# Optimization experiments

Hardware: AMD Instinct MI355X
Metric: run time of the kernel (lower is better)

The kernel has to match this reference:

```python
import jax, jax.numpy as jnp
import numpy as np

N, E, F, H = 50000, 1600000, 128, 128  # nodes, edges, input_nf, hidden_nf


def setup_inputs() -> dict:
    key = jax.random.key(0)
    ks = jax.random.split(key, 16)
    s = 0.05
    inp = {
        "h": jax.random.normal(ks[0], (N, F), jnp.float32),
        "coord": jax.random.normal(ks[1], (N, 3), jnp.float32),
        "edge_index": jax.random.randint(ks[2], (2, E), 0, N, jnp.int32),
        # edge_mlp: Linear(2F+1, H) -> SiLU -> Linear(H, H) -> SiLU
        "We1": jax.random.normal(ks[3], (2 * F + 1, H), jnp.float32) * s,
        "be1": jnp.zeros((H,), jnp.float32),
        "We2": jax.random.normal(ks[4], (H, H), jnp.float32) * s,
        "be2": jnp.zeros((H,), jnp.float32),
        # node_mlp: Linear(H+F, H) -> SiLU -> Linear(H, F)
        "Wn1": jax.random.normal(ks[5], (H + F, H), jnp.float32) * s,
        "bn1": jnp.zeros((H,), jnp.float32),
        "Wn2": jax.random.normal(ks[6], (H, F), jnp.float32) * s,
        "bn2": jnp.zeros((F,), jnp.float32),
        # coord_mlp: Linear(H, H) -> SiLU -> Linear(H, 1, bias=False) (xavier gain 0.001)
        "Wc1": jax.random.normal(ks[7], (H, H), jnp.float32) * s,
        "bc1": jnp.zeros((H,), jnp.float32),
        "Wc2": jax.random.normal(ks[8], (H, 1), jnp.float32) * 0.001,
    }
    return inp


def reference(h, coord, edge_index, We1, be1, We2, be2, Wn1, bn1, Wn2, bn2, Wc1, bc1, Wc2):
    row, col = edge_index[0], edge_index[1]
    n = h.shape[0]

    # coord2radial (normalize=False)
    coord_diff = coord[row] - coord[col]                      # [E, 3]
    radial = jnp.sum(coord_diff * coord_diff, axis=1, keepdims=True)  # [E, 1]

    # edge_model (attention=False, edge_attr=None)
    e_in = jnp.concatenate([h[row], h[col], radial], axis=1)  # [E, 2F+1]
    edge_feat = jax.nn.silu(jax.nn.silu(e_in @ We1 + be1) @ We2 + be2)  # [E, H]

    # coord_model (coords_agg='mean', reflection_equiv=True, tanh=False)
    phi = jax.nn.silu(edge_feat @ Wc1 + bc1) @ Wc2            # [E, 1]
    trans = coord_diff * phi                                   # [E, 3]
    agg_c = jax.ops.segment_sum(trans, row, num_segments=n)    # [N, 3]
    cnt = jax.ops.segment_sum(jnp.ones((trans.shape[0], 1), trans.dtype), row, num_segments=n)
    coord_out = coord + agg_c / jnp.maximum(cnt, 1.0)

    # node_model (node_attr=None, residual=True)
    agg_h = jax.ops.segment_sum(edge_feat, row, num_segments=n)  # [N, H]
    n_in = jnp.concatenate([h, agg_h], axis=1)                   # [N, F+H]
    h_out = h + (jax.nn.silu(n_in @ Wn1 + bn1) @ Wn2 + bn2)

    return h_out, coord_out
```

## Files before the change

kernel.cpp:

```cpp
#include <hip/hip_runtime.h>


typedef float f32x4 __attribute__((ext_vector_type(4)));
typedef short s16x8 __attribute__((ext_vector_type(8)));

#define NN   50000
#define EE   1600000
#define NHF  6400000
#define NBIN 50000
#define NT   25000

__device__ __forceinline__ unsigned short f2bf(float x){
  union { float f; unsigned int u; } v; v.f = x;
  unsigned int r = v.u + 0x7fffu + ((v.u >> 16) & 1u);
  return (unsigned short)(r >> 16);
}
__device__ __forceinline__ unsigned int pack2(float a, float b){
  unsigned int r;
  asm("v_cvt_pk_bf16_f32 %0, %1, %2" : "=v"(r) : "v"(a), "v"(b));
  return r;
}
__device__ __forceinline__ float silu_f(float x){
  return x * __builtin_amdgcn_rcpf(1.f + __expf(-x));
}
__device__ __forceinline__ float bflo(unsigned int u){ return __uint_as_float(u << 16); }
__device__ __forceinline__ float bfhi(unsigned int u){ return __uint_as_float(u & 0xffff0000u); }

__device__ __forceinline__ f32x4 mfma16(s16x8 a, s16x8 b, f32x4 c){
  return __builtin_amdgcn_mfma_f32_16x16x32_bf16(a, b, c, 0, 0, 0);
}

template<int CTRL> __device__ __forceinline__ float dppf(float x){
  return __int_as_float(__builtin_amdgcn_update_dpp(0, __float_as_int(x), CTRL, 0xF, 0xF, true));
}
template<int CTRL> __device__ __forceinline__ int dppi(int x){
  return __builtin_amdgcn_update_dpp(-1, x, CTRL, 0xF, 0xF, false);
}

__device__ __forceinline__ short* sptr(short* base, int fi, int slot){
  return (short*)((char*)base + (fi << 10) + (((slot << 4) ^ ((fi & 3) << 5))));
}

__global__ void pack_weights(const float* __restrict__ We1, const float* __restrict__ We2,
                             const float* __restrict__ Wc1, const float* __restrict__ Wn1,
                             const float* __restrict__ Wn2, short* __restrict__ wp)
{
  int b = blockIdx.x;
  int m = b >> 5, t = b & 31;
  int ft = t >> 2, ks = t & 3;
  int lane = threadIdx.x;
  const float* src;
  switch (m) {
    case 0: src = We1;            break;
    case 1: src = We1 + 128*128;  break;
    case 2: src = We2;            break;
    case 3: src = Wc1;            break;
    case 4: src = Wn1;            break;
    case 5: src = Wn1 + 128*128;  break;
    default: src = Wn2;           break;
  }
  short* dst = wp + m*16384 + (((ft<<2) + ks)*64 + lane)*8;
  int f  = (ft<<4) + (lane & 15);
  int kb = (ks<<5) + ((lane >> 4) << 3);
#pragma unroll
  for (int j = 0; j < 8; ++j)
    dst[j] = (short)f2bf(src[(kb + j)*128 + f]);
}

__global__ __launch_bounds__(256, 2)
void a1_kernel(const float* __restrict__ h32, const short* __restrict__ wp,
               unsigned short* __restrict__ A1)
{
  __shared__ short sA[16][64][8];
  const int tid = threadIdx.x, w = tid >> 6, lane = tid & 63;
  const int n0 = blockIdx.x << 6;
  const int el = tid >> 2, q = tid & 3;
  const int fi0 = ((el >> 4) << 2) + q, er = el & 15;
  {
    const int node = n0 + el;
    if (node < NN) {
      const float* hp = h32 + (size_t)node*128 + q*32;
#pragma unroll
      for (int lg = 0; lg < 4; ++lg) {
        f32x4 u = *(const f32x4*)(hp + lg*8);
        f32x4 v = *(const f32x4*)(hp + lg*8 + 4);
        uint4 o;
        o.x = pack2(u.x, u.y); o.y = pack2(u.z, u.w);
        o.z = pack2(v.x, v.y); o.w = pack2(v.z, v.w);
        *(uint4*)&sA[fi0][lg*16 + er][0] = o;
      }
    } else {
      s16x8 z = {};
#pragma unroll
      for (int lg = 0; lg < 4; ++lg) *(s16x8*)&sA[fi0][lg*16 + er][0] = z;
    }
  }
  __syncthreads();

  static const int wpm[3] = {0, 1, 4};
#pragma unroll
  for (int p = 0; p < 2; ++p) {
    s16x8 af[3][4];
#pragma unroll
    for (int j = 0; j < 3; ++j) {
      const int ftg = w*6 + p*3 + j;
      const int mi = ftg >> 3, fti = ftg & 7;
#pragma unroll
      for (int ks = 0; ks < 4; ++ks)
        af[j][ks] = *(const s16x8*)(wp + wpm[mi]*16384 + (((fti<<2) + ks)*64 + lane)*8);
    }
    f32x4 acc[3][4] = {};
#pragma unroll
    for (int et = 0; et < 4; ++et)
#pragma unroll
      for (int ks = 0; ks < 4; ++ks) {
        s16x8 b = *(const s16x8*)&sA[et*4+ks][lane][0];
#pragma unroll
        for (int j = 0; j < 3; ++j)
          acc[j][et] = mfma16(af[j][ks], b, acc[j][et]);
      }
#pragma unroll
    for (int j = 0; j < 3; ++j) {
      const int ftg = w*6 + p*3 + j;
#pragma unroll
      for (int et = 0; et < 4; ++et) {
        const int node = n0 + et*16 + (lane & 15);
        if (node < NN) {
          f32x4 a = acc[j][et];
          uint2 o; o.x = pack2(a.x, a.y); o.y = pack2(a.z, a.w);
          *(uint2*)(A1 + (size_t)node*384 + ftg*16 + ((lane >> 4) << 2)) = o;
        }
      }
    }
  }
}

__global__ void hist_k(const int* __restrict__ eidx, int* __restrict__ hist)
{
  int e = blockIdx.x*256 + threadIdx.x;
  if (e < EE) atomicAdd(&hist[eidx[e]], 1);
}

__global__ void scan_k(const int* __restrict__ hist, int* __restrict__ cur)
{
  __shared__ int s_a[256];
  const int t = threadIdx.x;
  const int lo = t * 196;
  const int hi = (lo + 196 < NBIN) ? lo + 196 : NBIN;
  int s = 0;
  for (int i = lo; i < hi; ++i) s += hist[i];
  s_a[t] = s;
  __syncthreads();
  int acc = s;
#pragma unroll
  for (int d = 1; d < 256; d <<= 1) {
    int u = (t >= d) ? s_a[t - d] : 0;
    __syncthreads();
    acc += u;
    s_a[t] = acc;
    __syncthreads();
  }
  int run = acc - s;
  for (int i = lo; i < hi; ++i) { cur[i] = run; run += hist[i]; }
}

__global__ void scatter_k(const int* __restrict__ eidx, int* __restrict__ cur,
                          int* __restrict__ perm)
{
  int e = blockIdx.x*256 + threadIdx.x;
  if (e < EE) {
    int p = atomicAdd(&cur[eidx[e]], 1);
    perm[p] = e;
  }
}

__global__ __launch_bounds__(256, 3)
void edge_kernel(const unsigned short* __restrict__ A1, const float* __restrict__ coord,
                 const int* __restrict__ eidx, const int* __restrict__ perm,
                 const short* __restrict__ wp,
                 const float* __restrict__ be1, const float* __restrict__ be2,
                 const float* __restrict__ bc1, const float* __restrict__ We1,
                 const float* __restrict__ Wc2,
                 float* __restrict__ aggh, float* __restrict__ aggc,
                 float* __restrict__ cntb)
{
  __shared__ short sAf[2][16*64*8];
  __shared__ float s_vec[5][128];
  __shared__ float s_rad[64];
  __shared__ float s_cd[64][3];
  __shared__ int   s_ri[64];
  __shared__ int   s_ci[64];
  __shared__ float s_phi[64];

  const int tid  = threadIdx.x;
  const int w    = tid >> 6, lane = tid & 63;
  const int ecol = lane & 15, rgrp = lane >> 4;

  if (tid < 128) {
    s_vec[0][tid] = be1[tid];
    s_vec[1][tid] = be2[tid];
    s_vec[2][tid] = bc1[tid];
    s_vec[3][tid] = We1[256*128 + tid];
    s_vec[4][tid] = Wc2[tid];
  }

  s16x8 wf2[2][4], wf3[2][4];
#pragma unroll
  for (int f2 = 0; f2 < 2; ++f2)
#pragma unroll
    for (int ks = 0; ks < 4; ++ks) {
      wf2[f2][ks] = *(const s16x8*)(wp + 2*16384 + ((((2*w+f2)<<2) + ks)*64 + lane)*8);
      wf3[f2][ks] = *(const s16x8*)(wp + 3*16384 + ((((2*w+f2)<<2) + ks)*64 + lane)*8);
    }

  short* sb0 = &sAf[0][0];
  short* sb1 = &sAf[1][0];

  const int tbeg = blockIdx.x * 13;
  const int tend = (tbeg + 13 < NT) ? tbeg + 13 : NT;

  for (int t = tbeg; t < tend; ++t) {
    const int e0 = t << 6;
    if (tid < 64) {
      int e = perm[e0 + tid];
      int r = eidx[e], c = eidx[EE + e];
      s_ri[tid] = r; s_ci[tid] = c;
      float ax = coord[3*r], ay = coord[3*r+1], az = coord[3*r+2];
      float bx = coord[3*c], by = coord[3*c+1], bz = coord[3*c+2];
      float dx = ax-bx, dy = ay-by, dz = az-bz;
      s_cd[tid][0] = dx; s_cd[tid][1] = dy; s_cd[tid][2] = dz;
      s_rad[tid] = dx*dx + dy*dy + dz*dz;
      s_phi[tid] = 0.f;
    }
    __syncthreads();

    {
      int rr[4], cc[4]; float rd[4];
#pragma unroll
      for (int et = 0; et < 4; ++et) {
        const int e_ = et*16 + ecol;
        rr[et] = s_ri[e_]; cc[et] = s_ci[e_]; rd[et] = s_rad[e_];
      }
      uint2 gr[2][4], gc[2][4];
#pragma unroll
      for (int f2 = 0; f2 < 2; ++f2) {
        const int f0 = (2*w+f2)*16 + (rgrp << 2);
#pragma unroll
        for (int et = 0; et < 4; ++et) {
          gr[f2][et] = *(const uint2*)(A1 + (size_t)rr[et]*384 + f0);
          gc[f2][et] = *(const uint2*)(A1 + (size_t)cc[et]*384 + 128 + f0);
        }
      }
#pragma unroll
      for (int f2 = 0; f2 < 2; ++f2) {
        const int f0 = (2*w+f2)*16 + (rgrp << 2);
        const int ks2 = f0 >> 5, lg2 = (f0 & 31) >> 3, j0 = f0 & 7;
        f32x4 w1c = *(const f32x4*)&s_vec[3][f0];
        f32x4 b1  = *(const f32x4*)&s_vec[0][f0];
#pragma unroll
        for (int et = 0; et < 4; ++et) {
          const uint2 r2v = gr[f2][et], c2v = gc[f2][et];
          f32x4 x;
          x.x = silu_f(bflo(r2v.x) + bflo(c2v.x) + rd[et]*w1c.x + b1.x);
          x.y = silu_f(bfhi(r2v.x) + bfhi(c2v.x) + rd[et]*w1c.y + b1.y);
          x.z = silu_f(bflo(r2v.y) + bflo(c2v.y) + rd[et]*w1c.z + b1.z);
          x.w = silu_f(bfhi(r2v.y) + bfhi(c2v.y) + rd[et]*w1c.w + b1.w);
          uint2 p; p.x = pack2(x.x, x.y); p.y = pack2(x.z, x.w);
          *(uint2*)((char*)sptr(sb0, et*4 + ks2, lg2*16 + ecol) + 2*j0) = p;
        }
      }
    }
    __syncthreads();

    f32x4 a2[2][4] = {};
#pragma unroll
    for (int et = 0; et < 4; ++et)
#pragma unroll
      for (int ks = 0; ks < 4; ++ks) {
        s16x8 b = *(const s16x8*)sptr(sb0, et*4+ks, lane);
        a2[0][et] = mfma16(wf2[0][ks], b, a2[0][et]);
        a2[1][et] = mfma16(wf2[1][ks], b, a2[1][et]);
      }
#pragma unroll
    for (int et = 0; et < 4; ++et) {
      const int r_l = s_ri[et*16 + ecol];
      f32x4 xx0, xx1;
#pragma unroll
      for (int f2 = 0; f2 < 2; ++f2) {
        const int f0 = (2*w+f2)*16 + (rgrp << 2);
        const int ks2 = f0 >> 5, lg2 = (f0 & 31) >> 3, j0 = f0 & 7;
        f32x4 b2 = *(const f32x4*)&s_vec[1][f0];
        f32x4 x = a2[f2][et];
        x.x = silu_f(x.x + b2.x); x.y = silu_f(x.y + b2.y);
        x.z = silu_f(x.z + b2.z); x.w = silu_f(x.w + b2.w);
        uint2 p; p.x = pack2(x.x, x.y); p.y = pack2(x.z, x.w);
        *(uint2*)((char*)sptr(sb1, et*4 + ks2, lg2*16 + ecol) + 2*j0) = p;
        if (f2 == 0) xx0 = x; else xx1 = x;
      }
#define SEG_ROUND(CTRL) { \
      int rn = dppi<CTRL>(r_l); \
      bool ok = (rn == r_l); \
      float u; \
      u = dppf<CTRL>(xx0.x); xx0.x += ok ? u : 0.f; \
      u = dppf<CTRL>(xx0.y); xx0.y += ok ? u : 0.f; \
      u = dppf<CTRL>(xx0.z); xx0.z += ok ? u : 0.f; \
      u = dppf<CTRL>(xx0.w); xx0.w += ok ? u : 0.f; \
      u = dppf<CTRL>(xx1.x); xx1.x += ok ? u : 0.f; \
      u = dppf<CTRL>(xx1.y); xx1.y += ok ? u : 0.f; \
      u = dppf<CTRL>(xx1.z); xx1.z += ok ? u : 0.f; \
      u = dppf<CTRL>(xx1.w); xx1.w += ok ? u : 0.f; }
      SEG_ROUND(0x101)
      SEG_ROUND(0x102)
      SEG_ROUND(0x104)
      SEG_ROUND(0x108)
#undef SEG_ROUND
      const int rprev = dppi<0x111>(r_l);
      if (rprev != r_l) {
        const int f0a = (2*w+0)*16 + (rgrp << 2);
        const int f0b = (2*w+1)*16 + (rgrp << 2);
        float* aga = aggh + (size_t)r_l*128 + f0a;
        float* agb = aggh + (size_t)r_l*128 + f0b;
        atomicAdd(aga+0, xx0.x); atomicAdd(aga+1, xx0.y);
        atomicAdd(aga+2, xx0.z); atomicAdd(aga+3, xx0.w);
        atomicAdd(agb+0, xx1.x); atomicAdd(agb+1, xx1.y);
        atomicAdd(agb+2, xx1.z); atomicAdd(agb+3, xx1.w);
      }
    }
    __syncthreads();

    f32x4 a3[2][4] = {};
#pragma unroll
    for (int et = 0; et < 4; ++et)
#pragma unroll
      for (int ks = 0; ks < 4; ++ks) {
        s16x8 b = *(const s16x8*)sptr(sb1, et*4+ks, lane);
        a3[0][et] = mfma16(wf3[0][ks], b, a3[0][et]);
        a3[1][et] = mfma16(wf3[1][ks], b, a3[1][et]);
      }
#pragma unroll
    for (int et = 0; et < 4; ++et) {
      float p = 0.f;
#pragma unroll
      for (int f2 = 0; f2 < 2; ++f2) {
        const int f0 = (2*w+f2)*16 + (rgrp << 2);
        f32x4 bc = *(const f32x4*)&s_vec[2][f0];
        f32x4 wc = *(const f32x4*)&s_vec[4][f0];
        f32x4 x = a3[f2][et];
        p += silu_f(x.x + bc.x)*wc.x + silu_f(x.y + bc.y)*wc.y
           + silu_f(x.z + bc.z)*wc.z + silu_f(x.w + bc.w)*wc.w;
      }
      p += __shfl_xor(p, 16);
      p += __shfl_xor(p, 32);
      if (rgrp == 0) atomicAdd(&s_phi[et*16 + ecol], p);
    }
    __syncthreads();

    if (tid < 64) {
      int r = s_ri[tid];
      float ph = s_phi[tid];
      float cx = s_cd[tid][0]*ph, cy = s_cd[tid][1]*ph, cz = s_cd[tid][2]*ph, c1 = 1.f;
#pragma unroll
      for (int d = 1; d < 64; d <<= 1) {
        const int sl = tid + d;
        int   r2 = __shfl(r,  sl, 64);
        float ux = __shfl(cx, sl, 64), uy = __shfl(cy, sl, 64);
        float uz = __shfl(cz, sl, 64), uw = __shfl(c1, sl, 64);
        if ((sl < 64) && (r2 == r)) { cx+=ux; cy+=uy; cz+=uz; c1+=uw; }
      }
      if (tid == 0 || s_ri[tid-1] != r) {
        atomicAdd(&aggc[3*r+0], cx); atomicAdd(&aggc[3*r+1], cy);
        atomicAdd(&aggc[3*r+2], cz); atomicAdd(&cntb[r], c1);
      }
    }
    __syncthreads();
  }
}

__global__ __launch_bounds__(256, 2)
void node_kernel(const unsigned short* __restrict__ A1, const float* __restrict__ h32,
                 const short* __restrict__ wp, const float* __restrict__ bn1,
                 const float* __restrict__ bn2, float* __restrict__ hout)
{
  __shared__ short sA[16][64][8];
  __shared__ float s_vec[2][128];
  const int tid  = threadIdx.x, w = tid >> 6, lane = tid & 63;
  const int ecol = lane & 15, rgrp = lane >> 4;
  if (tid < 128) { s_vec[0][tid] = bn1[tid]; s_vec[1][tid] = bn2[tid]; }

  s16x8 wfa[2][4], wfb[2][4];
#pragma unroll
  for (int f2 = 0; f2 < 2; ++f2)
#pragma unroll
    for (int ks = 0; ks < 4; ++ks) {
      wfa[f2][ks] = *(const s16x8*)(wp + 5*16384 + ((((2*w+f2)<<2) + ks)*64 + lane)*8);
      wfb[f2][ks] = *(const s16x8*)(wp + 6*16384 + ((((2*w+f2)<<2) + ks)*64 + lane)*8);
    }

  const int n0 = blockIdx.x << 6;
  const int el = tid >> 2, q = tid & 3;
  const int fi0 = ((el >> 4) << 2) + q, er = el & 15;
  {
    const int node = n0 + el;
    if (node < NN) {
      const float* ap = hout + (size_t)node*128 + q*32;
#pragma unroll
      for (int lg = 0; lg < 4; ++lg) {
        f32x4 u = *(const f32x4*)(ap + lg*8);
        f32x4 v = *(const f32x4*)(ap + lg*8 + 4);
        uint4 o;
        o.x = pack2(u.x, u.y); o.y = pack2(u.z, u.w);
        o.z = pack2(v.x, v.y); o.w = pack2(v.z, v.w);
        *(uint4*)&sA[fi0][lg*16 + er][0] = o;
      }
    } else {
      s16x8 z = {};
#pragma unroll
      for (int lg = 0; lg < 4; ++lg) *(s16x8*)&sA[fi0][lg*16 + er][0] = z;
    }
  }
  __syncthreads();

  f32x4 acc[2][4] = {};
#pragma unroll
  for (int et = 0; et < 4; ++et)
#pragma unroll
    for (int ks = 0; ks < 4; ++ks) {
      s16x8 ba = *(const s16x8*)&sA[et*4+ks][lane][0];
      acc[0][et] = mfma16(wfa[0][ks], ba, acc[0][et]);
      acc[1][et] = mfma16(wfa[1][ks], ba, acc[1][et]);
    }
  __syncthreads();

#pragma unroll
  for (int f2 = 0; f2 < 2; ++f2) {
    const int ft = 2*w + f2, f0 = ft*16 + (rgrp << 2);
    const int ks2 = f0 >> 5, lg2 = (f0 & 31) >> 3, j0 = f0 & 7;
    f32x4 b1 = *(const f32x4*)&s_vec[0][f0];
#pragma unroll
    for (int et = 0; et < 4; ++et) {
      const int node = n0 + et*16 + ecol;
      uint2 g = {0u, 0u};
      if (node < NN) g = *(const uint2*)(A1 + (size_t)node*384 + 256 + f0);
      f32x4 x = acc[f2][et];
      x.x = silu_f(x.x + bflo(g.x) + b1.x);
      x.y = silu_f(x.y + bfhi(g.x) + b1.y);
      x.z = silu_f(x.z + bflo(g.y) + b1.z);
      x.w = silu_f(x.w + bfhi(g.y) + b1.w);
      uint2 p; p.x = pack2(x.x, x.y); p.y = pack2(x.z, x.w);
      *(uint2*)&sA[et*4 + ks2][lg2*16 + ecol][j0] = p;
    }
  }
  __syncthreads();

  f32x4 a2[2][4] = {};
#pragma unroll
  for (int et = 0; et < 4; ++et)
#pragma unroll
    for (int ks = 0; ks < 4; ++ks) {
      s16x8 b = *(const s16x8*)&sA[et*4+ks][lane][0];
      a2[0][et] = mfma16(wfb[0][ks], b, a2[0][et]);
      a2[1][et] = mfma16(wfb[1][ks], b, a2[1][et]);
    }
#pragma unroll
  for (int f2 = 0; f2 < 2; ++f2) {
    const int f0 = (2*w+f2)*16 + (rgrp << 2);
    f32x4 b2 = *(const f32x4*)&s_vec[1][f0];
#pragma unroll
    for (int et = 0; et < 4; ++et) {
      const int node = n0 + et*16 + ecol;
      if (node < NN) {
        f32x4 hv = *(const f32x4*)(h32 + (size_t)node*128 + f0);
        f32x4 x = a2[f2][et];
        x.x += b2.x + hv.x; x.y += b2.y + hv.y;
        x.z += b2.z + hv.z; x.w += b2.w + hv.w;
        *(f32x4*)(hout + (size_t)node*128 + f0) = x;
      }
    }
  }
}

__global__ void coord_kernel(const float* __restrict__ coord, const float* __restrict__ aggc,
                             const float* __restrict__ cntb, float* __restrict__ out)
{
  int i = blockIdx.x*256 + threadIdx.x;
  if (i < NN) {
    float inv = __builtin_amdgcn_rcpf(fmaxf(cntb[i], 1.f));
    out[NHF + 3*i+0] = coord[3*i+0] + aggc[3*i+0]*inv;
    out[NHF + 3*i+1] = coord[3*i+1] + aggc[3*i+1]*inv;
    out[NHF + 3*i+2] = coord[3*i+2] + aggc[3*i+2]*inv;
  }
}

extern "C" void kernel_launch(void* const* d_in, const int* in_sizes, int n_in,
                              void* d_out, int out_size, void* d_ws, size_t ws_size,
                              hipStream_t stream)
{
  (void)in_sizes; (void)n_in; (void)out_size; (void)ws_size;
  const float* h    = (const float*)d_in[0];
  const float* crd  = (const float*)d_in[1];
  const int*   eidx = (const int*)  d_in[2];
  const float* We1  = (const float*)d_in[3];
  const float* be1  = (const float*)d_in[4];
  const float* We2  = (const float*)d_in[5];
  const float* be2  = (const float*)d_in[6];
  const float* Wn1  = (const float*)d_in[7];
  const float* bn1  = (const float*)d_in[8];
  const float* Wn2  = (const float*)d_in[9];
  const float* bn2  = (const float*)d_in[10];
  const float* Wc1  = (const float*)d_in[11];
  const float* bc1  = (const float*)d_in[12];
  const float* Wc2  = (const float*)d_in[13];
  float* out = (float*)d_out;
  char*  ws  = (char*)d_ws;

  short*          wp   = (short*)ws;
  unsigned short* A1   = (unsigned short*)(ws + 229376);
  float*          aggc = (float*)(ws + 38629376);
  float*          cntb = (float*)(ws + 39229376);
  int*            hist = (int*)  (ws + 39429376);
  int*            cur  = (int*)  (ws + 39629376);
  int*            perm = (int*)  (ws + 39829376);

  hipMemsetAsync(out, 0, (size_t)NHF*4, stream);
  hipMemsetAsync(ws + 38629376, 0, 800000, stream);
  hipMemsetAsync(ws + 39429376, 0, 200000, stream);

  pack_weights<<<dim3(224), dim3(64), 0, stream>>>(We1, We2, Wc1, Wn1, Wn2, wp);
  a1_kernel<<<dim3(782), dim3(256), 0, stream>>>(h, wp, A1);
  hist_k<<<dim3(6250), dim3(256), 0, stream>>>(eidx, hist);
  scan_k<<<dim3(1), dim3(256), 0, stream>>>(hist, cur);
  scatter_k<<<dim3(6250), dim3(256), 0, stream>>>(eidx, cur, perm);
  edge_kernel<<<dim3(1924), dim3(256), 0, stream>>>(A1, crd, eidx, perm, wp,
                                                    be1, be2, bc1, We1, Wc2,
                                                    out, aggc, cntb);
  node_kernel<<<dim3(782), dim3(256), 0, stream>>>(A1, h, wp, bn1, bn2, out);
  coord_kernel<<<dim3(196), dim3(256), 0, stream>>>(crd, aggc, cntb, out);
}
```

Baseline: 783.5 us.

## Merge small kernels, parallelize scan, and scatter row/col pairs directly

The histogram pass is folded into the A1 projection launch as extra blocks, and the coordinate update is folded into the node kernel the same way, which removes two launches. The single-block serial scan becomes a two-level parallel scan. The scatter now writes the sorted (row, col) pair directly instead of a permutation, so the edge kernel skips one dependent indirect load per edge. The segmented DPP reduction also swaps a conditional select for a multiply by a mask.

```diff
diff --git a/kernel.cpp b/kernel.cpp
--- a/kernel.cpp
+++ b/kernel.cpp
@@ -9,6 +9,8 @@
 #define NHF  6400000
 #define NBIN 50000
 #define NT   25000
+#define A1B  782
+#define NODB 782
 
 __device__ __forceinline__ unsigned short f2bf(float x){
   union { float f; unsigned int u; } v; v.f = x;
@@ -68,9 +70,15 @@
 }
 
 __global__ __launch_bounds__(256, 2)
-void a1_kernel(const float* __restrict__ h32, const short* __restrict__ wp,
-               unsigned short* __restrict__ A1)
-{
+void a1hist_kernel(const float* __restrict__ h32, const short* __restrict__ wp,
+                   unsigned short* __restrict__ A1,
+                   const int* __restrict__ eidx, int* __restrict__ hist)
+{
+  if (blockIdx.x >= A1B) {
+    int e = (blockIdx.x - A1B)*256 + threadIdx.x;
+    if (e < EE) atomicAdd(&hist[eidx[e]], 1);
+    return;
+  }
   __shared__ short sA[16][64][8];
   const int tid = threadIdx.x, w = tid >> 6, lane = tid & 63;
   const int n0 = blockIdx.x << 6;
@@ -135,49 +143,57 @@
   }
 }
 
-__global__ void hist_k(const int* __restrict__ eidx, int* __restrict__ hist)
-{
-  int e = blockIdx.x*256 + threadIdx.x;
-  if (e < EE) atomicAdd(&hist[eidx[e]], 1);
-}
-
-__global__ void scan_k(const int* __restrict__ hist, int* __restrict__ cur)
-{
-  __shared__ int s_a[256];
+__global__ void scanA(const int* __restrict__ hist, int* __restrict__ cur,
+                      int* __restrict__ btot)
+{
+  __shared__ int s[256];
   const int t = threadIdx.x;
-  const int lo = t * 196;
-  const int hi = (lo + 196 < NBIN) ? lo + 196 : NBIN;
-  int s = 0;
-  for (int i = lo; i < hi; ++i) s += hist[i];
-  s_a[t] = s;
-  __syncthreads();
-  int acc = s;
+  const int i = blockIdx.x*256 + t;
+  int v = (i < NBIN) ? hist[i] : 0;
+  s[t] = v; __syncthreads();
+  int acc = v;
 #pragma unroll
   for (int d = 1; d < 256; d <<= 1) {
-    int u = (t >= d) ? s_a[t - d] : 0;
-    __syncthreads();
-    acc += u;
-    s_a[t] = acc;
-    __syncthreads();
-  }
-  int run = acc - s;
-  for (int i = lo; i < hi; ++i) { cur[i] = run; run += hist[i]; }
+    int u = (t >= d) ? s[t - d] : 0;
+    __syncthreads();
+    acc += u; s[t] = acc;
+    __syncthreads();
+  }
+  if (i < NBIN) cur[i] = acc - v;
+  if (t == 255) btot[blockIdx.x] = acc;
+}
+__global__ void scanB(int* __restrict__ btot)
+{
+  __shared__ int s[256];
+  const int t = threadIdx.x;
+  int v = (t < 196) ? btot[t] : 0;
+  s[t] = v; __syncthreads();
+  int acc = v;
+#pragma unroll
+  for (int d = 1; d < 256; d <<= 1) {
+    int u = (t >= d) ? s[t - d] : 0;
+    __syncthreads();
+    acc += u; s[t] = acc;
+    __syncthreads();
+  }
+  if (t < 196) btot[t] = acc - v;
 }
 
 __global__ void scatter_k(const int* __restrict__ eidx, int* __restrict__ cur,
-                          int* __restrict__ perm)
+                          const int* __restrict__ btot, int2* __restrict__ rc)
 {
   int e = blockIdx.x*256 + threadIdx.x;
   if (e < EE) {
-    int p = atomicAdd(&cur[eidx[e]], 1);
-    perm[p] = e;
+    int r = eidx[e], c = eidx[EE + e];
+    int p = atomicAdd(&cur[r], 1) + btot[r >> 8];
+    int2 v; v.x = r; v.y = c;
+    rc[p] = v;
   }
 }
 
 __global__ __launch_bounds__(256, 3)
 void edge_kernel(const unsigned short* __restrict__ A1, const float* __restrict__ coord,
-                 const int* __restrict__ eidx, const int* __restrict__ perm,
-                 const short* __restrict__ wp,
+                 const int2* __restrict__ rc, const short* __restrict__ wp,
                  const float* __restrict__ be1, const float* __restrict__ be2,
                  const float* __restrict__ bc1, const float* __restrict__ We1,
                  const float* __restrict__ Wc2,
@@ -222,8 +238,8 @@
   for (int t = tbeg; t < tend; ++t) {
     const int e0 = t << 6;
     if (tid < 64) {
-      int e = perm[e0 + tid];
-      int r = eidx[e], c = eidx[EE + e];
+      int2 v = rc[e0 + tid];
+      int r = v.x, c = v.y;
       s_ri[tid] = r; s_ci[tid] = c;
       float ax = coord[3*r], ay = coord[3*r+1], az = coord[3*r+2];
       float bx = coord[3*c], by = coord[3*c+1], bz = coord[3*c+2];
@@ -259,12 +275,12 @@
         f32x4 b1  = *(const f32x4*)&s_vec[0][f0];
 #pragma unroll
         for (int et = 0; et < 4; ++et) {
-          const uint2 r2v = gr[f2][et], c2v = gc[f2][et];
+          const uint2 rv = gr[f2][et], cv = gc[f2][et];
           f32x4 x;
-          x.x = silu_f(bflo(r2v.x) + bflo(c2v.x) + rd[et]*w1c.x + b1.x);
-          x.y = silu_f(bfhi(r2v.x) + bfhi(c2v.x) + rd[et]*w1c.y + b1.y);
-          x.z = silu_f(bflo(r2v.y) + bflo(c2v.y) + rd[et]*w1c.z + b1.z);
-          x.w = silu_f(bfhi(r2v.y) + bfhi(c2v.y) + rd[et]*w1c.w + b1.w);
+          x.x = silu_f(bflo(rv.x) + bflo(cv.x) + rd[et]*w1c.x + b1.x);
+          x.y = silu_f(bfhi(rv.x) + bfhi(cv.x) + rd[et]*w1c.y + b1.y);
+          x.z = silu_f(bflo(rv.y) + bflo(cv.y) + rd[et]*w1c.z + b1.z);
+          x.w = silu_f(bfhi(rv.y) + bfhi(cv.y) + rd[et]*w1c.w + b1.w);
           uint2 p; p.x = pack2(x.x, x.y); p.y = pack2(x.z, x.w);
           *(uint2*)((char*)sptr(sb0, et*4 + ks2, lg2*16 + ecol) + 2*j0) = p;
         }
@@ -299,16 +315,15 @@
       }
 #define SEG_ROUND(CTRL) { \
       int rn = dppi<CTRL>(r_l); \
-      bool ok = (rn == r_l); \
-      float u; \
-      u = dppf<CTRL>(xx0.x); xx0.x += ok ? u : 0.f; \
-      u = dppf<CTRL>(xx0.y); xx0.y += ok ? u : 0.f; \
-      u = dppf<CTRL>(xx0.z); xx0.z += ok ? u : 0.f; \
-      u = dppf<CTRL>(xx0.w); xx0.w += ok ? u : 0.f; \
-      u = dppf<CTRL>(xx1.x); xx1.x += ok ? u : 0.f; \
-      u = dppf<CTRL>(xx1.y); xx1.y += ok ? u : 0.f; \
-      u = dppf<CTRL>(xx1.z); xx1.z += ok ? u : 0.f; \
-      u = dppf<CTRL>(xx1.w); xx1.w += ok ? u : 0.f; }
+      float m = (rn == r_l) ? 1.f : 0.f; \
+      xx0.x += dppf<CTRL>(xx0.x)*m; \
+      xx0.y += dppf<CTRL>(xx0.y)*m; \
+      xx0.z += dppf<CTRL>(xx0.z)*m; \
+      xx0.w += dppf<CTRL>(xx0.w)*m; \
+      xx1.x += dppf<CTRL>(xx1.x)*m; \
+      xx1.y += dppf<CTRL>(xx1.y)*m; \
+      xx1.z += dppf<CTRL>(xx1.z)*m; \
+      xx1.w += dppf<CTRL>(xx1.w)*m; }
       SEG_ROUND(0x101)
       SEG_ROUND(0x102)
       SEG_ROUND(0x104)
@@ -377,10 +392,22 @@
 }
 
 __global__ __launch_bounds__(256, 2)
-void node_kernel(const unsigned short* __restrict__ A1, const float* __restrict__ h32,
-                 const short* __restrict__ wp, const float* __restrict__ bn1,
-                 const float* __restrict__ bn2, float* __restrict__ hout)
-{
+void nodecoord_kernel(const unsigned short* __restrict__ A1, const float* __restrict__ h32,
+                      const short* __restrict__ wp, const float* __restrict__ bn1,
+                      const float* __restrict__ bn2, const float* __restrict__ coord,
+                      const float* __restrict__ aggc, const float* __restrict__ cntb,
+                      float* __restrict__ hout)
+{
+  if (blockIdx.x >= NODB) {
+    int i = (blockIdx.x - NODB)*256 + threadIdx.x;
+    if (i < NN) {
+      float inv = __builtin_amdgcn_rcpf(fmaxf(cntb[i], 1.f));
+      hout[NHF + 3*i+0] = coord[3*i+0] + aggc[3*i+0]*inv;
+      hout[NHF + 3*i+1] = coord[3*i+1] + aggc[3*i+1]*inv;
+      hout[NHF + 3*i+2] = coord[3*i+2] + aggc[3*i+2]*inv;
+    }
+    return;
+  }
   __shared__ short sA[16][64][8];
   __shared__ float s_vec[2][128];
   const int tid  = threadIdx.x, w = tid >> 6, lane = tid & 63;
@@ -476,18 +503,6 @@
         *(f32x4*)(hout + (size_t)node*128 + f0) = x;
       }
     }
-  }
-}
-
-__global__ void coord_kernel(const float* __restrict__ coord, const float* __restrict__ aggc,
-                             const float* __restrict__ cntb, float* __restrict__ out)
-{
-  int i = blockIdx.x*256 + threadIdx.x;
-  if (i < NN) {
-    float inv = __builtin_amdgcn_rcpf(fmaxf(cntb[i], 1.f));
-    out[NHF + 3*i+0] = coord[3*i+0] + aggc[3*i+0]*inv;
-    out[NHF + 3*i+1] = coord[3*i+1] + aggc[3*i+1]*inv;
-    out[NHF + 3*i+2] = coord[3*i+2] + aggc[3*i+2]*inv;
   }
 }
 
@@ -519,20 +534,21 @@
   float*          cntb = (float*)(ws + 39229376);
   int*            hist = (int*)  (ws + 39429376);
   int*            cur  = (int*)  (ws + 39629376);
-  int*            perm = (int*)  (ws + 39829376);
+  int*            btot = (int*)  (ws + 39829376);
+  int2*           rc   = (int2*) (ws + 39830400);
 
   hipMemsetAsync(out, 0, (size_t)NHF*4, stream);
   hipMemsetAsync(ws + 38629376, 0, 800000, stream);
   hipMemsetAsync(ws + 39429376, 0, 200000, stream);
 
   pack_weights<<<dim3(224), dim3(64), 0, stream>>>(We1, We2, Wc1, Wn1, Wn2, wp);
-  a1_kernel<<<dim3(782), dim3(256), 0, stream>>>(h, wp, A1);
-  hist_k<<<dim3(6250), dim3(256), 0, stream>>>(eidx, hist);
-  scan_k<<<dim3(1), dim3(256), 0, stream>>>(hist, cur);
-  scatter_k<<<dim3(6250), dim3(256), 0, stream>>>(eidx, cur, perm);
-  edge_kernel<<<dim3(1924), dim3(256), 0, stream>>>(A1, crd, eidx, perm, wp,
+  a1hist_kernel<<<dim3(A1B + 6250), dim3(256), 0, stream>>>(h, wp, A1, eidx, hist);
+  scanA<<<dim3(196), dim3(256), 0, stream>>>(hist, cur, btot);
+  scanB<<<dim3(1), dim3(256), 0, stream>>>(btot);
+  scatter_k<<<dim3(6250), dim3(256), 0, stream>>>(eidx, cur, btot, rc);
+  edge_kernel<<<dim3(1924), dim3(256), 0, stream>>>(A1, crd, rc, wp,
                                                     be1, be2, bc1, We1, Wc2,
                                                     out, aggc, cntb);
-  node_kernel<<<dim3(782), dim3(256), 0, stream>>>(A1, h, wp, bn1, bn2, out);
-  coord_kernel<<<dim3(196), dim3(256), 0, stream>>>(crd, aggc, cntb, out);
-}
+  nodecoord_kernel<<<dim3(NODB + 196), dim3(256), 0, stream>>>(A1, h, wp, bn1, bn2,
+                                                               crd, aggc, cntb, out);
+}
```

Result: faster. 650.6 us (-17.0%).
